# Kernel optimization log

Hardware: AMD Instinct MI355X
Metric: run time of the kernel (lower is better)

## Reference

```python
import jax, jax.numpy as jnp
import numpy as np

COMMITMENT_COST = 0.25
EMBEDDING_COST = 1.0


def setup_inputs() -> dict:
    key = jax.random.key(0)
    k1, k2 = jax.random.split(key)
    x = jax.random.normal(k1, (64, 1024, 64), dtype=jnp.float32)
    embeddings = jax.random.normal(k2, (1024, 64), dtype=jnp.float32)
    return {"x": x, "embeddings": embeddings}


def reference(x, embeddings):
    D = embeddings.shape[1]
    flat_x = x.reshape(-1, D)  # [N, D]
    distances = (
        jnp.sum(flat_x ** 2, axis=1, keepdims=True)
        + jnp.sum(embeddings ** 2, axis=1)
        - 2.0 * flat_x @ embeddings.T
    )
    encoding_indices = jnp.argmin(distances, axis=1)  # [N]
    quantized = embeddings[encoding_indices].reshape(x.shape)
    q_latent_loss = jnp.mean((quantized - jax.lax.stop_gradient(x)) ** 2) * EMBEDDING_COST
    e_latent_loss = jnp.mean((x - jax.lax.stop_gradient(quantized)) ** 2) * COMMITMENT_COST
    loss = q_latent_loss + e_latent_loss
    # Straight-through estimator
    quantized_st = x + jax.lax.stop_gradient(quantized - x)
    return (quantized_st, loss)
```

## Files before the change

### kernel.cpp

```cpp
#include <hip/hip_runtime.h>
#include <math.h>

#define NROWS 65536
#define D 64
#define K 1024
#define BR 128
#define EC 128
#define NCH (K / EC)
#define THREADS 256
#define TAU_S 0.005f
#define LOSS_SCALE (1.25f / (65536.0f * 64.0f))

typedef short bf16x8 __attribute__((ext_vector_type(8)));
typedef float f32x4 __attribute__((ext_vector_type(4)));

__device__ inline unsigned short f2bf(float f) {
    unsigned int u = __float_as_uint(f);
    unsigned int r = u + 0x7fffu + ((u >> 16) & 1u);
    return (unsigned short)(r >> 16);
}
__device__ inline float bf2f(unsigned short h) {
    return __uint_as_float(((unsigned int)h) << 16);
}
__device__ inline void cvt8(const float4& a, const float4& b, bf16x8& h, bf16x8& l) {
    float f[8] = {a.x, a.y, a.z, a.w, b.x, b.y, b.z, b.w};
#pragma unroll
    for (int j = 0; j < 8; ++j) {
        unsigned short hb = f2bf(f[j]);
        h[j] = (short)hb;
        l[j] = (short)f2bf(f[j] - bf2f(hb));
    }
}

__global__ void vq_prep(const float* __restrict__ E, float* __restrict__ C,
                        float* __restrict__ Ch,
                        bf16x8* __restrict__ Eh8, bf16x8* __restrict__ El8,
                        float* __restrict__ lossp, int* __restrict__ fcnt) {
    int k = blockIdx.x * blockDim.x + threadIdx.x;
    if (k == 0) { *lossp = 0.f; *fcnt = 0; }
    if (k >= K) return;
    const float4* ev = (const float4*)(E + (size_t)k * D);
    float s = 0.f;
#pragma unroll
    for (int u = 0; u < 8; ++u) {
        float4 a = ev[2 * u], b = ev[2 * u + 1];
        s = fmaf(a.x, a.x, s); s = fmaf(a.y, a.y, s);
        s = fmaf(a.z, a.z, s); s = fmaf(a.w, a.w, s);
        s = fmaf(b.x, b.x, s); s = fmaf(b.y, b.y, s);
        s = fmaf(b.z, b.z, s); s = fmaf(b.w, b.w, s);
        bf16x8 h, l;
        cvt8(a, b, h, l);
        Eh8[(size_t)k * 8 + u] = h;
        El8[(size_t)k * 8 + u] = l;
    }
    C[k] = s;
    Ch[k] = 0.5f * s;
}

__global__ __launch_bounds__(THREADS, 2) void vq_main(
    const float* __restrict__ X, const float* __restrict__ E,
    const float* __restrict__ Ch,
    const bf16x8* __restrict__ Eh8, const bf16x8* __restrict__ El8,
    int* __restrict__ bestk, int* __restrict__ flags, int* __restrict__ fcnt,
    float* __restrict__ out, float* __restrict__ lossp)
{
    __shared__ bf16x8 sEh8[EC * 8];
    __shared__ bf16x8 sEl8[EC * 8];
    __shared__ float  sCn[EC];
    __shared__ int    sIdx[BR];
    __shared__ float  sLoss[4];

    const int t    = threadIdx.x;
    const int w    = t >> 6;
    const int lane = t & 63;
    const int l15  = lane & 15;
    const int l4   = lane >> 4;

    const float4* Xg4 = (const float4*)X;

    bf16x8 ah[2][2], al[2][2];
#pragma unroll
    for (int rt = 0; rt < 2; ++rt) {
        size_t abase = ((size_t)blockIdx.x * BR + w * 32 + rt * 16 + l15) * 16;
#pragma unroll
        for (int kt = 0; kt < 2; ++kt) {
            float4 fa = Xg4[abase + kt * 8 + l4 * 2];
            float4 fb = Xg4[abase + kt * 8 + l4 * 2 + 1];
            cvt8(fa, fb, ah[rt][kt], al[rt][kt]);
        }
    }

    float m[2][4], m2[2][4]; int bk[2][4];
#pragma unroll
    for (int rt = 0; rt < 2; ++rt)
#pragma unroll
        for (int r = 0; r < 4; ++r) { m[rt][r] = -INFINITY; m2[rt][r] = -INFINITY; bk[rt][r] = 0; }

    bf16x8 rh[4], rl[4];
    float creg = 0.f;
#pragma unroll
    for (int p = 0; p < 4; ++p) {
        int S = p * 256 + t;
        rh[p] = Eh8[S];
        rl[p] = El8[S];
    }
    if (t < EC) creg = Ch[t];
#pragma unroll
    for (int p = 0; p < 4; ++p) {
        int S = p * 256 + t;
        int code = S >> 3, u8 = S & 7;
        int di = code * 8 + (u8 ^ (code & 7));
        sEh8[di] = rh[p];
        sEl8[di] = rl[p];
    }
    if (t < EC) sCn[t] = creg;
    __syncthreads();

    for (int ch = 0; ch < NCH; ++ch) {
        if (ch + 1 < NCH) {
#pragma unroll
            for (int p = 0; p < 4; ++p) {
                int S = p * 256 + t;
                rh[p] = Eh8[(size_t)(ch + 1) * (EC * 8) + S];
                rl[p] = El8[(size_t)(ch + 1) * (EC * 8) + S];
            }
            if (t < EC) creg = Ch[(ch + 1) * EC + t];
        }

#pragma unroll 2
        for (int t8 = 0; t8 < 8; ++t8) {
            int code = t8 * 16 + l15;
            int cs = code & 7;
            bf16x8 bh0 = sEh8[code * 8 + (l4 ^ cs)];
            bf16x8 bh1 = sEh8[code * 8 + ((4 + l4) ^ cs)];
            bf16x8 bl0 = sEl8[code * 8 + (l4 ^ cs)];
            bf16x8 bl1 = sEl8[code * 8 + ((4 + l4) ^ cs)];
            float ce2 = sCn[code];
            int kk = ch * EC + code;

#pragma unroll
            for (int rt = 0; rt < 2; ++rt) {
                f32x4 h = {0.f, 0.f, 0.f, 0.f}, x = {0.f, 0.f, 0.f, 0.f};
                h = __builtin_amdgcn_mfma_f32_16x16x32_bf16(ah[rt][0], bh0, h, 0, 0, 0);
                x = __builtin_amdgcn_mfma_f32_16x16x32_bf16(al[rt][0], bh0, x, 0, 0, 0);
                h = __builtin_amdgcn_mfma_f32_16x16x32_bf16(ah[rt][1], bh1, h, 0, 0, 0);
                x = __builtin_amdgcn_mfma_f32_16x16x32_bf16(al[rt][1], bh1, x, 0, 0, 0);
                x = __builtin_amdgcn_mfma_f32_16x16x32_bf16(ah[rt][0], bl0, x, 0, 0, 0);
                x = __builtin_amdgcn_mfma_f32_16x16x32_bf16(ah[rt][1], bl1, x, 0, 0, 0);
#pragma unroll
                for (int r = 0; r < 4; ++r) {
                    float v = (h[r] + x[r]) - ce2;
                    m2[rt][r] = fmaxf(m2[rt][r], fminf(m[rt][r], v));
                    bk[rt][r] = (v > m[rt][r]) ? kk : bk[rt][r];
                    m[rt][r]  = fmaxf(m[rt][r], v);
                }
            }
        }
        __syncthreads();
        if (ch + 1 < NCH) {
#pragma unroll
            for (int p = 0; p < 4; ++p) {
                int S = p * 256 + t;
                int code = S >> 3, u8 = S & 7;
                int di = code * 8 + (u8 ^ (code & 7));
                sEh8[di] = rh[p];
                sEl8[di] = rl[p];
            }
            if (t < EC) sCn[t] = creg;
        }
        __syncthreads();
    }

#pragma unroll
    for (int rt = 0; rt < 2; ++rt)
#pragma unroll
        for (int r = 0; r < 4; ++r) {
            float mm = m[rt][r], mm2 = m2[rt][r]; int kk = bk[rt][r];
#pragma unroll
            for (int off = 1; off < 16; off <<= 1) {
                float om  = __shfl_xor(mm,  off, 64);
                float om2 = __shfl_xor(mm2, off, 64);
                int   ok  = __shfl_xor(kk,  off, 64);
                mm2 = fmaxf(fmaxf(mm2, om2), fminf(mm, om));
                if (om > mm || (om == mm && ok < kk)) { mm = om; kk = ok; }
            }
            if (l15 == 0) {
                int lr = w * 32 + rt * 16 + l4 * 4 + r;
                sIdx[lr] = kk;
                if (mm - mm2 < TAU_S) {
                    int pos = atomicAdd(fcnt, 1);
                    flags[pos] = blockIdx.x * BR + lr;
                }
            }
        }
    __syncthreads();

    {
        int row = t >> 1, half = t & 1;
        int kb = sIdx[row];
        size_t grow = (size_t)blockIdx.x * BR + row;
        if (half == 0) bestk[grow] = kb;
        const float4* eq   = (const float4*)E + (size_t)kb * 16;
        const float4* xrow = Xg4 + grow * 16;
        float4* orow = (float4*)out + grow * 16;
        float ls = 0.f;
#pragma unroll
        for (int j = 0; j < 8; ++j) {
            int u = half * 8 + j;
            float4 qv = eq[u];
            float4 xv = xrow[u];
            orow[u] = qv;
            float dx = qv.x - xv.x; ls = fmaf(dx, dx, ls);
            float dy = qv.y - xv.y; ls = fmaf(dy, dy, ls);
            float dz = qv.z - xv.z; ls = fmaf(dz, dz, ls);
            float dw = qv.w - xv.w; ls = fmaf(dw, dw, ls);
        }
#pragma unroll
        for (int off = 32; off > 0; off >>= 1) ls += __shfl_down(ls, off, 64);
        if (lane == 0) sLoss[w] = ls;
        __syncthreads();
        if (t == 0)
            atomicAdd(lossp, (sLoss[0] + sLoss[1] + sLoss[2] + sLoss[3]) * LOSS_SCALE);
    }
}

__global__ __launch_bounds__(64) void vq_fix(
    const float* __restrict__ X, const float* __restrict__ E,
    const float* __restrict__ C,
    const int* __restrict__ bestk, const int* __restrict__ flags,
    const int* __restrict__ fcnt,
    float* __restrict__ out, float* __restrict__ lossp)
{
    __shared__ float4 sx4[16];
    const int lane = threadIdx.x;
    const float4* Eg4 = (const float4*)E;
    int nf = *fcnt;

    for (int i = blockIdx.x; i < nf; i += gridDim.x) {
        int row = flags[i];
        float xd = X[(size_t)row * D + lane];
        ((float*)sx4)[lane] = xd;
        float rx = xd * xd;
#pragma unroll
        for (int off = 1; off < 64; off <<= 1) rx += __shfl_xor(rx, off, 64);
        __syncthreads();

        float mm = INFINITY; int kb = 0;
        for (int jj = 0; jj < K / 64; ++jj) {
            int kk = jj * 64 + lane;
            const float4* er = Eg4 + (size_t)kk * 16;
            float a0 = 0.f, a1 = 0.f, a2 = 0.f, a3 = 0.f;
#pragma unroll
            for (int p = 0; p < 16; p += 4) {
                float4 xv0 = sx4[p],     e0 = er[p];
                float4 xv1 = sx4[p + 1], e1 = er[p + 1];
                float4 xv2 = sx4[p + 2], e2 = er[p + 2];
                float4 xv3 = sx4[p + 3], e3 = er[p + 3];
                a0 = fmaf(xv0.x, e0.x, a0); a0 = fmaf(xv0.y, e0.y, a0);
                a0 = fmaf(xv0.z, e0.z, a0); a0 = fmaf(xv0.w, e0.w, a0);
                a1 = fmaf(xv1.x, e1.x, a1); a1 = fmaf(xv1.y, e1.y, a1);
                a1 = fmaf(xv1.z, e1.z, a1); a1 = fmaf(xv1.w, e1.w, a1);
                a2 = fmaf(xv2.x, e2.x, a2); a2 = fmaf(xv2.y, e2.y, a2);
                a2 = fmaf(xv2.z, e2.z, a2); a2 = fmaf(xv2.w, e2.w, a2);
                a3 = fmaf(xv3.x, e3.x, a3); a3 = fmaf(xv3.y, e3.y, a3);
                a3 = fmaf(xv3.z, e3.z, a3); a3 = fmaf(xv3.w, e3.w, a3);
            }
            float dot = (a0 + a1) + (a2 + a3);
            float dd = fmaf(-2.f, dot, rx + C[kk]);
            if (dd < mm) { mm = dd; kb = kk; }
        }
#pragma unroll
        for (int off = 1; off < 64; off <<= 1) {
            float om = __shfl_xor(mm, off, 64);
            int   ok = __shfl_xor(kb, off, 64);
            if (om < mm || (om == mm && ok < kb)) { mm = om; kb = ok; }
        }
        int ko = bestk[row];
        if (kb != ko) {
            if (lane < 16) {
                float4 qn = Eg4[(size_t)kb * 16 + lane];
                float4 qo = Eg4[(size_t)ko * 16 + lane];
                float4 xv = sx4[lane];
                float dl = 0.f;
                float a, b2;
                a = qn.x - xv.x; b2 = qo.x - xv.x; dl += a * a - b2 * b2;
                a = qn.y - xv.y; b2 = qo.y - xv.y; dl += a * a - b2 * b2;
                a = qn.z - xv.z; b2 = qo.z - xv.z; dl += a * a - b2 * b2;
                a = qn.w - xv.w; b2 = qo.w - xv.w; dl += a * a - b2 * b2;
#pragma unroll
                for (int off = 1; off < 16; off <<= 1) dl += __shfl_xor(dl, off, 16);
                ((float4*)out)[(size_t)row * 16 + lane] = qn;
                if (lane == 0) atomicAdd(lossp, dl * LOSS_SCALE);
            }
        }
        __syncthreads();
    }
}

extern "C" void kernel_launch(void* const* d_in, const int* in_sizes, int n_in,
                              void* d_out, int out_size, void* d_ws, size_t ws_size,
                              hipStream_t stream) {
    const float* X = (const float*)d_in[0];
    const float* E = (const float*)d_in[1];
    float* out   = (float*)d_out;
    float* lossp = out + (size_t)NROWS * D;

    float* C     = (float*)d_ws;
    float* Ch    = (float*)d_ws + 1024;
    int*   bestk = (int*)d_ws + 2048;
    int*   flags = (int*)d_ws + 2048 + 65536;
    int*   fcnt  = (int*)d_ws + 2048 + 2 * 65536;
    bf16x8* Eh8  = (bf16x8*)((int*)d_ws + 2048 + 2 * 65536 + 4);
    bf16x8* El8  = Eh8 + (size_t)K * 8;

    vq_prep<<<(K + 255) / 256, 256, 0, stream>>>(E, C, Ch, Eh8, El8, lossp, fcnt);

    vq_main<<<NROWS / BR, THREADS, 0, stream>>>(
        X, E, Ch, Eh8, El8, bestk, flags, fcnt, out, lossp);

    vq_fix<<<512, 64, 0, stream>>>(X, E, C, bestk, flags, fcnt, out, lossp);
}
```

Baseline: 71.55 us.

## Fuse near-tie fixup into main kernel and double-buffer pre-swizzled codebook

Prep now writes the codebook in the pre-swizzled hi/lo bf16 layout main uses, so main copies it straight into LDS. Main double-buffers the chunks, so each chunk needs one barrier instead of two. It preloads all half-norms into LDS and seeds the MFMA accumulators with -|e|^2/2. It interleaves four independent accumulators per group under raised wave priority. The separate fixup kernel is gone: near-tie rows are collected in LDS and recomputed exactly in fp32 inside the same block before output. This removes one launch plus the global flag and bestk traffic, but adds a serial fp32 tail inside each block.

```diff
diff --git a/kernel.cpp b/kernel.cpp
--- a/kernel.cpp
+++ b/kernel.cpp
@@ -6,7 +6,7 @@
 #define K 1024
 #define BR 128
 #define EC 128
-#define NCH (K / EC)
+#define NCH 8
 #define THREADS 256
 #define TAU_S 0.005f
 #define LOSS_SCALE (1.25f / (65536.0f * 64.0f))
@@ -32,42 +32,45 @@
     }
 }
 
-__global__ void vq_prep(const float* __restrict__ E, float* __restrict__ C,
-                        float* __restrict__ Ch,
-                        bf16x8* __restrict__ Eh8, bf16x8* __restrict__ El8,
-                        float* __restrict__ lossp, int* __restrict__ fcnt) {
+#define MFMA __builtin_amdgcn_mfma_f32_16x16x32_bf16
+
+__global__ void vq_prep(const float* __restrict__ E, float* __restrict__ Ch,
+                        bf16x8* __restrict__ Eswz, float* __restrict__ lossp) {
     int k = blockIdx.x * blockDim.x + threadIdx.x;
-    if (k == 0) { *lossp = 0.f; *fcnt = 0; }
+    if (k == 0) *lossp = 0.f;
     if (k >= K) return;
     const float4* ev = (const float4*)(E + (size_t)k * D);
+    float4 v4[16];
     float s = 0.f;
 #pragma unroll
-    for (int u = 0; u < 8; ++u) {
-        float4 a = ev[2 * u], b = ev[2 * u + 1];
-        s = fmaf(a.x, a.x, s); s = fmaf(a.y, a.y, s);
-        s = fmaf(a.z, a.z, s); s = fmaf(a.w, a.w, s);
-        s = fmaf(b.x, b.x, s); s = fmaf(b.y, b.y, s);
-        s = fmaf(b.z, b.z, s); s = fmaf(b.w, b.w, s);
+    for (int p = 0; p < 16; ++p) {
+        float4 v = ev[p];
+        v4[p] = v;
+        s = fmaf(v.x, v.x, s); s = fmaf(v.y, v.y, s);
+        s = fmaf(v.z, v.z, s); s = fmaf(v.w, v.w, s);
+    }
+    Ch[k] = 0.5f * s;
+    int ch = k >> 7, c = k & 127, cs = c & 7;
+    size_t base = (size_t)ch * 2048 + c * 8;
+#pragma unroll
+    for (int u8 = 0; u8 < 8; ++u8) {
         bf16x8 h, l;
-        cvt8(a, b, h, l);
-        Eh8[(size_t)k * 8 + u] = h;
-        El8[(size_t)k * 8 + u] = l;
-    }
-    C[k] = s;
-    Ch[k] = 0.5f * s;
+        cvt8(v4[2 * u8], v4[2 * u8 + 1], h, l);
+        Eswz[base + (u8 ^ cs)] = h;
+        Eswz[base + 1024 + (u8 ^ cs)] = l;
+    }
 }
 
 __global__ __launch_bounds__(THREADS, 2) void vq_main(
     const float* __restrict__ X, const float* __restrict__ E,
-    const float* __restrict__ Ch,
-    const bf16x8* __restrict__ Eh8, const bf16x8* __restrict__ El8,
-    int* __restrict__ bestk, int* __restrict__ flags, int* __restrict__ fcnt,
+    const float* __restrict__ Chg, const bf16x8* __restrict__ Eswz,
     float* __restrict__ out, float* __restrict__ lossp)
 {
-    __shared__ bf16x8 sEh8[EC * 8];
-    __shared__ bf16x8 sEl8[EC * 8];
-    __shared__ float  sCn[EC];
+    __shared__ bf16x8 sBuf[2][2048];
+    __shared__ float  sCh[K];
     __shared__ int    sIdx[BR];
+    __shared__ int    sFlag[BR];
+    __shared__ int    sNf;
     __shared__ float  sLoss[4];
 
     const int t    = threadIdx.x;
@@ -75,98 +78,114 @@
     const int lane = t & 63;
     const int l15  = lane & 15;
     const int l4   = lane >> 4;
+    const int cs   = l15 & 7;
+    const int o0   = l4 ^ cs;
+    const int o1   = (4 + l4) ^ cs;
 
     const float4* Xg4 = (const float4*)X;
+    const float4* Eg4 = (const float4*)E;
+
+    if (t == 0) sNf = 0;
+#pragma unroll
+    for (int p = 0; p < 4; ++p) sCh[p * 256 + t] = Chg[p * 256 + t];
 
     bf16x8 ah[2][2], al[2][2];
 #pragma unroll
     for (int rt = 0; rt < 2; ++rt) {
-        size_t abase = ((size_t)blockIdx.x * BR + w * 32 + rt * 16 + l15) * 16;
+        size_t ab = ((size_t)blockIdx.x * BR + w * 32 + rt * 16 + l15) * 16;
 #pragma unroll
         for (int kt = 0; kt < 2; ++kt) {
-            float4 fa = Xg4[abase + kt * 8 + l4 * 2];
-            float4 fb = Xg4[abase + kt * 8 + l4 * 2 + 1];
+            float4 fa = Xg4[ab + kt * 8 + l4 * 2];
+            float4 fb = Xg4[ab + kt * 8 + l4 * 2 + 1];
             cvt8(fa, fb, ah[rt][kt], al[rt][kt]);
         }
     }
 
+    bf16x8 rs[8];
+#pragma unroll
+    for (int p = 0; p < 8; ++p) rs[p] = Eswz[p * 256 + t];
+#pragma unroll
+    for (int p = 0; p < 8; ++p) sBuf[0][p * 256 + t] = rs[p];
+    __syncthreads();
+
     float m[2][4], m2[2][4]; int bk[2][4];
 #pragma unroll
     for (int rt = 0; rt < 2; ++rt)
 #pragma unroll
         for (int r = 0; r < 4; ++r) { m[rt][r] = -INFINITY; m2[rt][r] = -INFINITY; bk[rt][r] = 0; }
 
-    bf16x8 rh[4], rl[4];
-    float creg = 0.f;
-#pragma unroll
-    for (int p = 0; p < 4; ++p) {
-        int S = p * 256 + t;
-        rh[p] = Eh8[S];
-        rl[p] = El8[S];
-    }
-    if (t < EC) creg = Ch[t];
-#pragma unroll
-    for (int p = 0; p < 4; ++p) {
-        int S = p * 256 + t;
-        int code = S >> 3, u8 = S & 7;
-        int di = code * 8 + (u8 ^ (code & 7));
-        sEh8[di] = rh[p];
-        sEl8[di] = rl[p];
-    }
-    if (t < EC) sCn[t] = creg;
-    __syncthreads();
-
     for (int ch = 0; ch < NCH; ++ch) {
+        const int cur = ch & 1;
         if (ch + 1 < NCH) {
 #pragma unroll
-            for (int p = 0; p < 4; ++p) {
-                int S = p * 256 + t;
-                rh[p] = Eh8[(size_t)(ch + 1) * (EC * 8) + S];
-                rl[p] = El8[(size_t)(ch + 1) * (EC * 8) + S];
-            }
-            if (t < EC) creg = Ch[(ch + 1) * EC + t];
-        }
-
-#pragma unroll 2
-        for (int t8 = 0; t8 < 8; ++t8) {
-            int code = t8 * 16 + l15;
-            int cs = code & 7;
-            bf16x8 bh0 = sEh8[code * 8 + (l4 ^ cs)];
-            bf16x8 bh1 = sEh8[code * 8 + ((4 + l4) ^ cs)];
-            bf16x8 bl0 = sEl8[code * 8 + (l4 ^ cs)];
-            bf16x8 bl1 = sEl8[code * 8 + ((4 + l4) ^ cs)];
-            float ce2 = sCn[code];
-            int kk = ch * EC + code;
-
-#pragma unroll
-            for (int rt = 0; rt < 2; ++rt) {
-                f32x4 h = {0.f, 0.f, 0.f, 0.f}, x = {0.f, 0.f, 0.f, 0.f};
-                h = __builtin_amdgcn_mfma_f32_16x16x32_bf16(ah[rt][0], bh0, h, 0, 0, 0);
-                x = __builtin_amdgcn_mfma_f32_16x16x32_bf16(al[rt][0], bh0, x, 0, 0, 0);
-                h = __builtin_amdgcn_mfma_f32_16x16x32_bf16(ah[rt][1], bh1, h, 0, 0, 0);
-                x = __builtin_amdgcn_mfma_f32_16x16x32_bf16(al[rt][1], bh1, x, 0, 0, 0);
-                x = __builtin_amdgcn_mfma_f32_16x16x32_bf16(ah[rt][0], bl0, x, 0, 0, 0);
-                x = __builtin_amdgcn_mfma_f32_16x16x32_bf16(ah[rt][1], bl1, x, 0, 0, 0);
-#pragma unroll
-                for (int r = 0; r < 4; ++r) {
-                    float v = (h[r] + x[r]) - ce2;
-                    m2[rt][r] = fmaxf(m2[rt][r], fminf(m[rt][r], v));
-                    bk[rt][r] = (v > m[rt][r]) ? kk : bk[rt][r];
-                    m[rt][r]  = fmaxf(m[rt][r], v);
-                }
-            }
-        }
-        __syncthreads();
+            for (int p = 0; p < 8; ++p)
+                rs[p] = Eswz[(size_t)(ch + 1) * 2048 + p * 256 + t];
+        }
+        const bf16x8* __restrict__ bufH = sBuf[cur];
+        const bf16x8* __restrict__ bufL = sBuf[cur] + 1024;
+
+#pragma unroll
+        for (int g = 0; g < 4; ++g) {
+            const int c0 = g * 32 + l15;
+            const int c1 = c0 + 16;
+            float ce0 = sCh[ch * EC + c0];
+            float ce1 = sCh[ch * EC + c1];
+            bf16x8 bh00 = bufH[c0 * 8 + o0];
+            bf16x8 bh01 = bufH[c0 * 8 + o1];
+            bf16x8 bl00 = bufL[c0 * 8 + o0];
+            bf16x8 bl01 = bufL[c0 * 8 + o1];
+            bf16x8 bh10 = bufH[c1 * 8 + o0];
+            bf16x8 bh11 = bufH[c1 * 8 + o1];
+            bf16x8 bl10 = bufL[c1 * 8 + o0];
+            bf16x8 bl11 = bufL[c1 * 8 + o1];
+
+            f32x4 a00 = {-ce0, -ce0, -ce0, -ce0};
+            f32x4 a01 = {-ce0, -ce0, -ce0, -ce0};
+            f32x4 a10 = {-ce1, -ce1, -ce1, -ce1};
+            f32x4 a11 = {-ce1, -ce1, -ce1, -ce1};
+
+            __builtin_amdgcn_s_setprio(1);
+            a00 = MFMA(ah[0][0], bh00, a00, 0, 0, 0); a01 = MFMA(ah[1][0], bh00, a01, 0, 0, 0);
+            a10 = MFMA(ah[0][0], bh10, a10, 0, 0, 0); a11 = MFMA(ah[1][0], bh10, a11, 0, 0, 0);
+            a00 = MFMA(ah[0][1], bh01, a00, 0, 0, 0); a01 = MFMA(ah[1][1], bh01, a01, 0, 0, 0);
+            a10 = MFMA(ah[0][1], bh11, a10, 0, 0, 0); a11 = MFMA(ah[1][1], bh11, a11, 0, 0, 0);
+            a00 = MFMA(al[0][0], bh00, a00, 0, 0, 0); a01 = MFMA(al[1][0], bh00, a01, 0, 0, 0);
+            a10 = MFMA(al[0][0], bh10, a10, 0, 0, 0); a11 = MFMA(al[1][0], bh10, a11, 0, 0, 0);
+            a00 = MFMA(al[0][1], bh01, a00, 0, 0, 0); a01 = MFMA(al[1][1], bh01, a01, 0, 0, 0);
+            a10 = MFMA(al[0][1], bh11, a10, 0, 0, 0); a11 = MFMA(al[1][1], bh11, a11, 0, 0, 0);
+            a00 = MFMA(ah[0][0], bl00, a00, 0, 0, 0); a01 = MFMA(ah[1][0], bl00, a01, 0, 0, 0);
+            a10 = MFMA(ah[0][0], bl10, a10, 0, 0, 0); a11 = MFMA(ah[1][0], bl10, a11, 0, 0, 0);
+            a00 = MFMA(ah[0][1], bl01, a00, 0, 0, 0); a01 = MFMA(ah[1][1], bl01, a01, 0, 0, 0);
+            a10 = MFMA(ah[0][1], bl11, a10, 0, 0, 0); a11 = MFMA(ah[1][1], bl11, a11, 0, 0, 0);
+            __builtin_amdgcn_s_setprio(0);
+
+            const int k0 = ch * EC + c0;
+            const int k1 = ch * EC + c1;
+#pragma unroll
+            for (int r = 0; r < 4; ++r) {
+                float v;
+                v = a00[r];
+                m2[0][r] = fmaxf(m2[0][r], fminf(m[0][r], v));
+                bk[0][r] = (v > m[0][r]) ? k0 : bk[0][r];
+                m[0][r]  = fmaxf(m[0][r], v);
+                v = a01[r];
+                m2[1][r] = fmaxf(m2[1][r], fminf(m[1][r], v));
+                bk[1][r] = (v > m[1][r]) ? k0 : bk[1][r];
+                m[1][r]  = fmaxf(m[1][r], v);
+                v = a10[r];
+                m2[0][r] = fmaxf(m2[0][r], fminf(m[0][r], v));
+                bk[0][r] = (v > m[0][r]) ? k1 : bk[0][r];
+                m[0][r]  = fmaxf(m[0][r], v);
+                v = a11[r];
+                m2[1][r] = fmaxf(m2[1][r], fminf(m[1][r], v));
+                bk[1][r] = (v > m[1][r]) ? k1 : bk[1][r];
+                m[1][r]  = fmaxf(m[1][r], v);
+            }
+        }
+
         if (ch + 1 < NCH) {
 #pragma unroll
-            for (int p = 0; p < 4; ++p) {
-                int S = p * 256 + t;
-                int code = S >> 3, u8 = S & 7;
-                int di = code * 8 + (u8 ^ (code & 7));
-                sEh8[di] = rh[p];
-                sEl8[di] = rl[p];
-            }
-            if (t < EC) sCn[t] = creg;
+            for (int p = 0; p < 8; ++p) sBuf[cur ^ 1][p * 256 + t] = rs[p];
         }
         __syncthreads();
     }
@@ -188,19 +207,59 @@
                 int lr = w * 32 + rt * 16 + l4 * 4 + r;
                 sIdx[lr] = kk;
                 if (mm - mm2 < TAU_S) {
-                    int pos = atomicAdd(fcnt, 1);
-                    flags[pos] = blockIdx.x * BR + lr;
+                    int pos = atomicAdd(&sNf, 1);
+                    sFlag[pos] = lr;
                 }
             }
         }
+    __syncthreads();
+
+    {
+        int nf = sNf;
+        for (int i = w; i < nf; i += 4) {
+            int lr = sFlag[i];
+            size_t grow = (size_t)blockIdx.x * BR + lr;
+            const float4* xr = Xg4 + grow * 16;
+            float bs = -INFINITY; int bki = 0;
+#pragma unroll 1
+            for (int jj = 0; jj < 16; ++jj) {
+                int kq = jj * 64 + lane;
+                const float4* er = Eg4 + (size_t)kq * 16;
+                float a0 = 0.f, a1 = 0.f, a2 = 0.f, a3 = 0.f;
+#pragma unroll
+                for (int p = 0; p < 16; p += 4) {
+                    float4 xv0 = xr[p],     e0 = er[p];
+                    float4 xv1 = xr[p + 1], e1 = er[p + 1];
+                    float4 xv2 = xr[p + 2], e2 = er[p + 2];
+                    float4 xv3 = xr[p + 3], e3 = er[p + 3];
+                    a0 = fmaf(xv0.x, e0.x, a0); a0 = fmaf(xv0.y, e0.y, a0);
+                    a0 = fmaf(xv0.z, e0.z, a0); a0 = fmaf(xv0.w, e0.w, a0);
+                    a1 = fmaf(xv1.x, e1.x, a1); a1 = fmaf(xv1.y, e1.y, a1);
+                    a1 = fmaf(xv1.z, e1.z, a1); a1 = fmaf(xv1.w, e1.w, a1);
+                    a2 = fmaf(xv2.x, e2.x, a2); a2 = fmaf(xv2.y, e2.y, a2);
+                    a2 = fmaf(xv2.z, e2.z, a2); a2 = fmaf(xv2.w, e2.w, a2);
+                    a3 = fmaf(xv3.x, e3.x, a3); a3 = fmaf(xv3.y, e3.y, a3);
+                    a3 = fmaf(xv3.z, e3.z, a3); a3 = fmaf(xv3.w, e3.w, a3);
+                }
+                float sv = ((a0 + a1) + (a2 + a3)) - sCh[kq];
+                if (sv > bs) { bs = sv; bki = kq; }
+            }
+#pragma unroll
+            for (int off = 1; off < 64; off <<= 1) {
+                float ob = __shfl_xor(bs, off, 64);
+                int  okk = __shfl_xor(bki, off, 64);
+                if (ob > bs || (ob == bs && okk < bki)) { bs = ob; bki = okk; }
+            }
+            if (lane == 0) sIdx[lr] = bki;
+        }
+    }
     __syncthreads();
 
     {
         int row = t >> 1, half = t & 1;
         int kb = sIdx[row];
         size_t grow = (size_t)blockIdx.x * BR + row;
-        if (half == 0) bestk[grow] = kb;
-        const float4* eq   = (const float4*)E + (size_t)kb * 16;
+        const float4* eq   = Eg4 + (size_t)kb * 16;
         const float4* xrow = Xg4 + grow * 16;
         float4* orow = (float4*)out + grow * 16;
         float ls = 0.f;
@@ -224,79 +283,6 @@
     }
 }
 
-__global__ __launch_bounds__(64) void vq_fix(
-    const float* __restrict__ X, const float* __restrict__ E,
-    const float* __restrict__ C,
-    const int* __restrict__ bestk, const int* __restrict__ flags,
-    const int* __restrict__ fcnt,
-    float* __restrict__ out, float* __restrict__ lossp)
-{
-    __shared__ float4 sx4[16];
-    const int lane = threadIdx.x;
-    const float4* Eg4 = (const float4*)E;
-    int nf = *fcnt;
-
-    for (int i = blockIdx.x; i < nf; i += gridDim.x) {
-        int row = flags[i];
-        float xd = X[(size_t)row * D + lane];
-        ((float*)sx4)[lane] = xd;
-        float rx = xd * xd;
-#pragma unroll
-        for (int off = 1; off < 64; off <<= 1) rx += __shfl_xor(rx, off, 64);
-        __syncthreads();
-
-        float mm = INFINITY; int kb = 0;
-        for (int jj = 0; jj < K / 64; ++jj) {
-            int kk = jj * 64 + lane;
-            const float4* er = Eg4 + (size_t)kk * 16;
-            float a0 = 0.f, a1 = 0.f, a2 = 0.f, a3 = 0.f;
-#pragma unroll
-            for (int p = 0; p < 16; p += 4) {
-                float4 xv0 = sx4[p],     e0 = er[p];
-                float4 xv1 = sx4[p + 1], e1 = er[p + 1];
-                float4 xv2 = sx4[p + 2], e2 = er[p + 2];
-                float4 xv3 = sx4[p + 3], e3 = er[p + 3];
-                a0 = fmaf(xv0.x, e0.x, a0); a0 = fmaf(xv0.y, e0.y, a0);
-                a0 = fmaf(xv0.z, e0.z, a0); a0 = fmaf(xv0.w, e0.w, a0);
-                a1 = fmaf(xv1.x, e1.x, a1); a1 = fmaf(xv1.y, e1.y, a1);
-                a1 = fmaf(xv1.z, e1.z, a1); a1 = fmaf(xv1.w, e1.w, a1);
-                a2 = fmaf(xv2.x, e2.x, a2); a2 = fmaf(xv2.y, e2.y, a2);
-                a2 = fmaf(xv2.z, e2.z, a2); a2 = fmaf(xv2.w, e2.w, a2);
-                a3 = fmaf(xv3.x, e3.x, a3); a3 = fmaf(xv3.y, e3.y, a3);
-                a3 = fmaf(xv3.z, e3.z, a3); a3 = fmaf(xv3.w, e3.w, a3);
-            }
-            float dot = (a0 + a1) + (a2 + a3);
-            float dd = fmaf(-2.f, dot, rx + C[kk]);
-            if (dd < mm) { mm = dd; kb = kk; }
-        }
-#pragma unroll
-        for (int off = 1; off < 64; off <<= 1) {
-            float om = __shfl_xor(mm, off, 64);
-            int   ok = __shfl_xor(kb, off, 64);
-            if (om < mm || (om == mm && ok < kb)) { mm = om; kb = ok; }
-        }
-        int ko = bestk[row];
-        if (kb != ko) {
-            if (lane < 16) {
-                float4 qn = Eg4[(size_t)kb * 16 + lane];
-                float4 qo = Eg4[(size_t)ko * 16 + lane];
-                float4 xv = sx4[lane];
-                float dl = 0.f;
-                float a, b2;
-                a = qn.x - xv.x; b2 = qo.x - xv.x; dl += a * a - b2 * b2;
-                a = qn.y - xv.y; b2 = qo.y - xv.y; dl += a * a - b2 * b2;
-                a = qn.z - xv.z; b2 = qo.z - xv.z; dl += a * a - b2 * b2;
-                a = qn.w - xv.w; b2 = qo.w - xv.w; dl += a * a - b2 * b2;
-#pragma unroll
-                for (int off = 1; off < 16; off <<= 1) dl += __shfl_xor(dl, off, 16);
-                ((float4*)out)[(size_t)row * 16 + lane] = qn;
-                if (lane == 0) atomicAdd(lossp, dl * LOSS_SCALE);
-            }
-        }
-        __syncthreads();
-    }
-}
-
 extern "C" void kernel_launch(void* const* d_in, const int* in_sizes, int n_in,
                               void* d_out, int out_size, void* d_ws, size_t ws_size,
                               hipStream_t stream) {
@@ -305,18 +291,11 @@
     float* out   = (float*)d_out;
     float* lossp = out + (size_t)NROWS * D;
 
-    float* C     = (float*)d_ws;
-    float* Ch    = (float*)d_ws + 1024;
-    int*   bestk = (int*)d_ws + 2048;
-    int*   flags = (int*)d_ws + 2048 + 65536;
-    int*   fcnt  = (int*)d_ws + 2048 + 2 * 65536;
-    bf16x8* Eh8  = (bf16x8*)((int*)d_ws + 2048 + 2 * 65536 + 4);
-    bf16x8* El8  = Eh8 + (size_t)K * 8;
-
-    vq_prep<<<(K + 255) / 256, 256, 0, stream>>>(E, C, Ch, Eh8, El8, lossp, fcnt);
+    float*  Ch   = (float*)d_ws;
+    bf16x8* Eswz = (bf16x8*)((float*)d_ws + 1024);
+
+    vq_prep<<<(K + 255) / 256, 256, 0, stream>>>(E, Ch, Eswz, lossp);
 
     vq_main<<<NROWS / BR, THREADS, 0, stream>>>(
-        X, E, Ch, Eh8, El8, bestk, flags, fcnt, out, lossp);
-
-    vq_fix<<<512, 64, 0, stream>>>(X, E, C, bestk, flags, fcnt, out, lossp);
-}
+        X, E, Ch, Eswz, out, lossp);
+}
```

Result: no change. 72.34 us (+1.1%).
